# Performance work log

Measured on AMD Instinct MI355X. Metric: run time of the kernel, lower is better.

The kernel has to match this reference:

```python
import jax, jax.numpy as jnp
import numpy as np

TEMPERATURE = 1.0  # config['attention_temperature']


def setup_inputs() -> dict:
    key = jax.random.key(0)
    k1, k2, k3 = jax.random.split(key, 3)
    B, S, F, D = 4, 4096, 33, 64
    x = jax.random.normal(k1, (B, S, F), dtype=jnp.float32)
    Wq = jax.random.normal(k2, (F, D), dtype=jnp.float32) / np.sqrt(F)
    bq = jnp.zeros((D,), dtype=jnp.float32)
    Wk = jax.random.normal(k3, (F, D), dtype=jnp.float32) / np.sqrt(F)
    bk = jnp.zeros((D,), dtype=jnp.float32)
    return {"x": x, "Wq": Wq, "bq": bq, "Wk": Wk, "bk": bk}


def reference(x, Wq, bq, Wk, bk):
    # queries/keys: affine projections of the same input (MLP with one layer)
    q = x @ Wq + bq                              # [B, S, D]
    k = x @ Wk + bk                              # [B, S, D]
    qkt = jnp.einsum("bsd,btd->bst", q, k)       # [B, S, S]
    # non-standard normalization: divide each row by its max, scale by temperature
    row_max = jnp.max(qkt, axis=-1, keepdims=True)
    dist = jax.nn.softmax(TEMPERATURE * qkt / row_max, axis=-1)
    return dist
```

## Files before the change

kernel.cpp:

```cpp
#include <hip/hip_runtime.h>
#include <hip/hip_bf16.h>

typedef __bf16 bf16_t;
typedef __bf16 bf16x8 __attribute__((ext_vector_type(8)));
typedef float f32x4 __attribute__((ext_vector_type(4)));
typedef __fp16 f16x2 __attribute__((ext_vector_type(2)));

#define BATCH 4
#define SEQ 4096
#define FIN 33
#define DIM 64
#define LOG2E 1.4426950408889634f

__device__ __forceinline__ float dexp2(float x) { return __builtin_amdgcn_exp2f(x); }
__device__ __forceinline__ unsigned pk(float a, float b)
{ return __builtin_bit_cast(unsigned, __builtin_amdgcn_cvt_pkrtz(a, b)); }
__device__ __forceinline__ f16x2 uph(unsigned u)
{ return __builtin_bit_cast(f16x2, u); }
__device__ __forceinline__ float f16lo(unsigned u)
{ return (float)uph(u)[0]; }

__device__ __forceinline__ f32x4 mm2(bf16x8 a0, bf16x8 a1, bf16x8 b0, bf16x8 b1)
{
    f32x4 acc = {0.f, 0.f, 0.f, 0.f};
    acc = __builtin_amdgcn_mfma_f32_16x16x32_bf16(a0, b0, acc, 0, 0, 0);
    acc = __builtin_amdgcn_mfma_f32_16x16x32_bf16(a1, b1, acc, 0, 0, 0);
    return acc;
}

__global__ __launch_bounds__(256) void qk_proj_kernel(
    const float* __restrict__ x, const float* __restrict__ Wq,
    const float* __restrict__ bq, const float* __restrict__ Wk,
    const float* __restrict__ bk,
    bf16_t* __restrict__ qout, bf16_t* __restrict__ kout)
{
    __shared__ float sWq[FIN * DIM];
    __shared__ float sWk[FIN * DIM];
    __shared__ float sb[2 * DIM];
    const int t = threadIdx.x;
    for (int i = t; i < FIN * DIM; i += 256) { sWq[i] = Wq[i]; sWk[i] = Wk[i]; }
    if (t < DIM) { sb[t] = bq[t]; sb[DIM + t] = bk[t]; }
    __syncthreads();

    const int row = blockIdx.x * 4 + (t >> 6);
    const int d   = t & 63;
    const float* xr = x + (size_t)row * FIN;
    float qacc = sb[d], kacc = sb[DIM + d];
#pragma unroll
    for (int f = 0; f < FIN; ++f) {
        const float xv = xr[f];
        qacc += xv * sWq[f * DIM + d];
        kacc += xv * sWk[f * DIM + d];
    }
    qout[(size_t)row * DIM + d] = (bf16_t)qacc;
    kout[(size_t)row * DIM + d] = (bf16_t)kacc;
}

#define LDK(ct, h) (*reinterpret_cast<const bf16x8*>(kw + (size_t)(ct) * 16 * DIM + (h) * 32))

__global__ __launch_bounds__(256) void mz_kernel(
    const bf16_t* __restrict__ qg, const bf16_t* __restrict__ kg,
    float* __restrict__ cMg, float* __restrict__ invZg)
{
    const int wg   = blockIdx.x;
    const int b    = wg >> 7;
    const int t    = threadIdx.x;
    const int w    = t >> 6;
    const int l    = t & 63;
    const int lr   = l & 15;
    const int kg4  = l >> 4;
    const int col0 = w << 10;

    const bf16_t* kw = kg + ((size_t)b * SEQ + col0 + lr) * DIM + kg4 * 8;
    const bf16_t* qb = qg + (size_t)(wg * 32) * DIM;

    const bf16x8 qa0 = *reinterpret_cast<const bf16x8*>(qb + lr * DIM + kg4 * 8);
    const bf16x8 qa1 = *reinterpret_cast<const bf16x8*>(qb + lr * DIM + 32 + kg4 * 8);
    const bf16x8 qb0 = *reinterpret_cast<const bf16x8*>(qb + (16 + lr) * DIM + kg4 * 8);
    const bf16x8 qb1 = *reinterpret_cast<const bf16x8*>(qb + (16 + lr) * DIM + 32 + kg4 * 8);

    __shared__ float redM[4][32];
    __shared__ float redZ[4][32];

    float vA[4] = {-3.4e38f, -3.4e38f, -3.4e38f, -3.4e38f};
    float vB[4] = {-3.4e38f, -3.4e38f, -3.4e38f, -3.4e38f};
    {
        bf16x8 p0a = LDK(0, 0), p0b = LDK(0, 1);
        bf16x8 p1a = LDK(1, 0), p1b = LDK(1, 1);
#pragma unroll 4
        for (int ct = 0; ct < 64; ct += 2) {
            f32x4 aA = mm2(qa0, qa1, p0a, p0b);
            f32x4 aB = mm2(qb0, qb1, p0a, p0b);
            if (ct + 2 < 64) { p0a = LDK(ct + 2, 0); p0b = LDK(ct + 2, 1); }
#pragma unroll
            for (int j = 0; j < 4; ++j) { vA[j] = fmaxf(vA[j], aA[j]); vB[j] = fmaxf(vB[j], aB[j]); }
            f32x4 cA = mm2(qa0, qa1, p1a, p1b);
            f32x4 cB = mm2(qb0, qb1, p1a, p1b);
            if (ct + 3 < 64) { p1a = LDK(ct + 3, 0); p1b = LDK(ct + 3, 1); }
#pragma unroll
            for (int j = 0; j < 4; ++j) { vA[j] = fmaxf(vA[j], cA[j]); vB[j] = fmaxf(vB[j], cB[j]); }
        }
    }
#pragma unroll
    for (int m = 1; m < 16; m <<= 1) {
#pragma unroll
        for (int j = 0; j < 4; ++j) {
            vA[j] = fmaxf(vA[j], __shfl_xor(vA[j], m, 64));
            vB[j] = fmaxf(vB[j], __shfl_xor(vB[j], m, 64));
        }
    }
    if (lr == 0) {
#pragma unroll
        for (int j = 0; j < 4; ++j) {
            redM[w][kg4 * 4 + j]      = vA[j];
            redM[w][16 + kg4 * 4 + j] = vB[j];
        }
    }
    __syncthreads();
    float cMA[4], cMB[4];
#pragma unroll
    for (int j = 0; j < 4; ++j) {
        const int rA = kg4 * 4 + j, rB = 16 + kg4 * 4 + j;
        float mA = redM[0][rA], mB = redM[0][rB];
#pragma unroll
        for (int ww = 1; ww < 4; ++ww) { mA = fmaxf(mA, redM[ww][rA]); mB = fmaxf(mB, redM[ww][rB]); }
        cMA[j] = LOG2E / mA;
        cMB[j] = LOG2E / mB;
    }

    float zA[4] = {0.f, 0.f, 0.f, 0.f};
    float zB[4] = {0.f, 0.f, 0.f, 0.f};
    {
        bf16x8 p0a = LDK(0, 0), p0b = LDK(0, 1);
        bf16x8 p1a = LDK(1, 0), p1b = LDK(1, 1);
#pragma unroll 4
        for (int ct = 0; ct < 64; ct += 2) {
            f32x4 aA = mm2(qa0, qa1, p0a, p0b);
            f32x4 aB = mm2(qb0, qb1, p0a, p0b);
            if (ct + 2 < 64) { p0a = LDK(ct + 2, 0); p0b = LDK(ct + 2, 1); }
#pragma unroll
            for (int j = 0; j < 4; ++j) {
                zA[j] += dexp2(fmaf(aA[j], cMA[j], -LOG2E));
                zB[j] += dexp2(fmaf(aB[j], cMB[j], -LOG2E));
            }
            f32x4 cA = mm2(qa0, qa1, p1a, p1b);
            f32x4 cB = mm2(qb0, qb1, p1a, p1b);
            if (ct + 3 < 64) { p1a = LDK(ct + 3, 0); p1b = LDK(ct + 3, 1); }
#pragma unroll
            for (int j = 0; j < 4; ++j) {
                zA[j] += dexp2(fmaf(cA[j], cMA[j], -LOG2E));
                zB[j] += dexp2(fmaf(cB[j], cMB[j], -LOG2E));
            }
        }
    }
#pragma unroll
    for (int m = 1; m < 16; m <<= 1) {
#pragma unroll
        for (int j = 0; j < 4; ++j) {
            zA[j] += __shfl_xor(zA[j], m, 64);
            zB[j] += __shfl_xor(zB[j], m, 64);
        }
    }
    if (lr == 0) {
#pragma unroll
        for (int j = 0; j < 4; ++j) {
            redZ[w][kg4 * 4 + j]      = zA[j];
            redZ[w][16 + kg4 * 4 + j] = zB[j];
        }
    }
    __syncthreads();
    if (t < 32) {
        float mm = redM[0][t], zz = redZ[0][t];
#pragma unroll
        for (int ww = 1; ww < 4; ++ww) { mm = fmaxf(mm, redM[ww][t]); zz += redZ[ww][t]; }
        cMg[wg * 32 + t]   = LOG2E / mm;
        invZg[wg * 32 + t] = 1.0f / zz;
    }
}

__global__ __launch_bounds__(256) void p_kernel(
    const bf16_t* __restrict__ qg, const bf16_t* __restrict__ kg,
    const float* __restrict__ cMg, const float* __restrict__ invZg,
    float* __restrict__ out)
{
    const int w     = threadIdx.x >> 6;
    const int chunk = blockIdx.x * 4 + w;
    const int rb    = chunk >> 4;
    const int cc    = chunk & 15;
    const int b     = rb >> 8;
    const int l     = threadIdx.x & 63;
    const int lr    = l & 15;
    const int kg4   = l >> 4;
    const int col0  = cc << 8;
    const int sr    = l >> 3;

    __shared__ uint2 sS[4][4][256];
    uint2* const sp = &sS[w][kg4][lr];

    float cM[4];
#pragma unroll
    for (int j = 0; j < 4; ++j) cM[j] = cMg[rb * 16 + kg4 * 4 + j];
    const float iz0 = invZg[rb * 16 + sr];
    const float iz1 = invZg[rb * 16 + sr + 8];

    const bf16_t* qb = qg + (size_t)(rb * 16) * DIM;
    const bf16x8 a0 = *reinterpret_cast<const bf16x8*>(qb + lr * DIM + kg4 * 8);
    const bf16x8 a1 = *reinterpret_cast<const bf16x8*>(qb + lr * DIM + 32 + kg4 * 8);
    const bf16_t* kw = kg + ((size_t)b * SEQ + col0 + lr) * DIM + kg4 * 8;

    {
        bf16x8 p0a = LDK(0, 0), p0b = LDK(0, 1);
        bf16x8 p1a = LDK(1, 0), p1b = LDK(1, 1);
#pragma unroll
        for (int ct = 0; ct < 16; ct += 2) {
            f32x4 acc0 = mm2(a0, a1, p0a, p0b);
            if (ct + 2 < 16) { p0a = LDK(ct + 2, 0); p0b = LDK(ct + 2, 1); }
            {
                const float e0 = dexp2(fmaf(acc0[0], cM[0], -LOG2E));
                const float e1 = dexp2(fmaf(acc0[1], cM[1], -LOG2E));
                const float e2 = dexp2(fmaf(acc0[2], cM[2], -LOG2E));
                const float e3 = dexp2(fmaf(acc0[3], cM[3], -LOG2E));
                sp[ct * 16] = make_uint2(pk(e0, e1), pk(e2, e3));
            }
            f32x4 acc1 = mm2(a0, a1, p1a, p1b);
            if (ct + 3 < 16) { p1a = LDK(ct + 3, 0); p1b = LDK(ct + 3, 1); }
            {
                const float e0 = dexp2(fmaf(acc1[0], cM[0], -LOG2E));
                const float e1 = dexp2(fmaf(acc1[1], cM[1], -LOG2E));
                const float e2 = dexp2(fmaf(acc1[2], cM[2], -LOG2E));
                const float e3 = dexp2(fmaf(acc1[3], cM[3], -LOG2E));
                sp[(ct + 1) * 16] = make_uint2(pk(e0, e1), pk(e2, e3));
            }
        }
    }
    asm volatile("s_waitcnt lgkmcnt(0)" ::: "memory");

    {
        const int  cl  = (l & 7) * 4;
        const unsigned hsh = (unsigned)((sr & 1) * 16);
        const bool hiw = (sr & 2) != 0;
        const int  g0  = sr >> 2;
        float* ob0 = out + ((size_t)(rb * 16 + sr)) * SEQ + col0;
        float* ob1 = ob0 + (size_t)8 * SEQ;
#pragma unroll
        for (int it = 0; it < 8; ++it) {
            const int c = it * 32 + cl;
            const uint4 A0 = *reinterpret_cast<const uint4*>(&sS[w][g0][c]);
            const uint4 B0 = *reinterpret_cast<const uint4*>(&sS[w][g0][c + 2]);
            const uint4 A1 = *reinterpret_cast<const uint4*>(&sS[w][g0 + 2][c]);
            const uint4 B1 = *reinterpret_cast<const uint4*>(&sS[w][g0 + 2][c + 2]);
            f32x4 v0, v1;
            v0[0] = f16lo((hiw ? A0.y : A0.x) >> hsh);
            v0[1] = f16lo((hiw ? A0.w : A0.z) >> hsh);
            v0[2] = f16lo((hiw ? B0.y : B0.x) >> hsh);
            v0[3] = f16lo((hiw ? B0.w : B0.z) >> hsh);
            v1[0] = f16lo((hiw ? A1.y : A1.x) >> hsh);
            v1[1] = f16lo((hiw ? A1.w : A1.z) >> hsh);
            v1[2] = f16lo((hiw ? B1.y : B1.x) >> hsh);
            v1[3] = f16lo((hiw ? B1.w : B1.z) >> hsh);
            *reinterpret_cast<f32x4*>(ob0 + c) = v0 * iz0;
            *reinterpret_cast<f32x4*>(ob1 + c) = v1 * iz1;
        }
    }
}

extern "C" void kernel_launch(void* const* d_in, const int* in_sizes, int n_in,
                              void* d_out, int out_size, void* d_ws, size_t ws_size,
                              hipStream_t stream)
{
    const float* x  = (const float*)d_in[0];
    const float* Wq = (const float*)d_in[1];
    const float* bq = (const float*)d_in[2];
    const float* Wk = (const float*)d_in[3];
    const float* bk = (const float*)d_in[4];
    float* out = (float*)d_out;

    bf16_t* qws = (bf16_t*)d_ws;
    bf16_t* kws = qws + (size_t)BATCH * SEQ * DIM;
    float*  cMg = (float*)(kws + (size_t)BATCH * SEQ * DIM);
    float*  iZg = cMg + (size_t)BATCH * SEQ;

    qk_proj_kernel<<<(BATCH * SEQ) / 4, 256, 0, stream>>>(x, Wq, bq, Wk, bk, qws, kws);
    mz_kernel<<<BATCH * (SEQ / 32), 256, 0, stream>>>(qws, kws, cMg, iZg);
    p_kernel<<<BATCH * (SEQ / 16) * 16 / 4, 256, 0, stream>>>(qws, kws, cMg, iZg, out);
}
```

Before: 154.3 us.

## Halve rows per stats block, widen output blocks, and swizzle block order across XCDs

The max/sum kernel now handles 16 query rows per workgroup instead of 32, which doubles the grid and roughly halves per-block MFMA work. The output kernel uses 512-thread blocks that each cover half a row block (2048 columns across 8 waves). Its write-back now reads from shared memory across waves after a block barrier, so each wave writes two full contiguous rows. Both kernels remap blockIdx so consecutive blocks land on different XCDs while adjacent row blocks stay together for K reuse in L2. The trade-off is more K reloads in the stats pass and a full-block barrier in the output pass.

Result: slower. 208.4 us (+35.1%).

```diff
diff --git a/kernel.cpp b/kernel.cpp
--- a/kernel.cpp
+++ b/kernel.cpp
@@ -62,8 +62,8 @@
     const bf16_t* __restrict__ qg, const bf16_t* __restrict__ kg,
     float* __restrict__ cMg, float* __restrict__ invZg)
 {
-    const int wg   = blockIdx.x;
-    const int b    = wg >> 7;
+    const int wg   = ((blockIdx.x & 7) << 7) | (blockIdx.x >> 3);
+    const int b    = wg >> 8;
     const int t    = threadIdx.x;
     const int w    = t >> 6;
     const int l    = t & 63;
@@ -72,141 +72,110 @@
     const int col0 = w << 10;
 
     const bf16_t* kw = kg + ((size_t)b * SEQ + col0 + lr) * DIM + kg4 * 8;
-    const bf16_t* qb = qg + (size_t)(wg * 32) * DIM;
-
-    const bf16x8 qa0 = *reinterpret_cast<const bf16x8*>(qb + lr * DIM + kg4 * 8);
-    const bf16x8 qa1 = *reinterpret_cast<const bf16x8*>(qb + lr * DIM + 32 + kg4 * 8);
-    const bf16x8 qb0 = *reinterpret_cast<const bf16x8*>(qb + (16 + lr) * DIM + kg4 * 8);
-    const bf16x8 qb1 = *reinterpret_cast<const bf16x8*>(qb + (16 + lr) * DIM + 32 + kg4 * 8);
-
-    __shared__ float redM[4][32];
-    __shared__ float redZ[4][32];
-
-    float vA[4] = {-3.4e38f, -3.4e38f, -3.4e38f, -3.4e38f};
-    float vB[4] = {-3.4e38f, -3.4e38f, -3.4e38f, -3.4e38f};
+    const bf16_t* qb = qg + (size_t)(wg * 16) * DIM;
+
+    const bf16x8 a0 = *reinterpret_cast<const bf16x8*>(qb + lr * DIM + kg4 * 8);
+    const bf16x8 a1 = *reinterpret_cast<const bf16x8*>(qb + lr * DIM + 32 + kg4 * 8);
+
+    __shared__ float redM[4][16];
+    __shared__ float redZ[4][16];
+
+    float vmax[4] = {-3.4e38f, -3.4e38f, -3.4e38f, -3.4e38f};
     {
         bf16x8 p0a = LDK(0, 0), p0b = LDK(0, 1);
         bf16x8 p1a = LDK(1, 0), p1b = LDK(1, 1);
 #pragma unroll 4
         for (int ct = 0; ct < 64; ct += 2) {
-            f32x4 aA = mm2(qa0, qa1, p0a, p0b);
-            f32x4 aB = mm2(qb0, qb1, p0a, p0b);
+            f32x4 acc0 = mm2(a0, a1, p0a, p0b);
             if (ct + 2 < 64) { p0a = LDK(ct + 2, 0); p0b = LDK(ct + 2, 1); }
 #pragma unroll
-            for (int j = 0; j < 4; ++j) { vA[j] = fmaxf(vA[j], aA[j]); vB[j] = fmaxf(vB[j], aB[j]); }
-            f32x4 cA = mm2(qa0, qa1, p1a, p1b);
-            f32x4 cB = mm2(qb0, qb1, p1a, p1b);
+            for (int j = 0; j < 4; ++j) vmax[j] = fmaxf(vmax[j], acc0[j]);
+            f32x4 acc1 = mm2(a0, a1, p1a, p1b);
             if (ct + 3 < 64) { p1a = LDK(ct + 3, 0); p1b = LDK(ct + 3, 1); }
 #pragma unroll
-            for (int j = 0; j < 4; ++j) { vA[j] = fmaxf(vA[j], cA[j]); vB[j] = fmaxf(vB[j], cB[j]); }
+            for (int j = 0; j < 4; ++j) vmax[j] = fmaxf(vmax[j], acc1[j]);
         }
     }
 #pragma unroll
     for (int m = 1; m < 16; m <<= 1) {
 #pragma unroll
-        for (int j = 0; j < 4; ++j) {
-            vA[j] = fmaxf(vA[j], __shfl_xor(vA[j], m, 64));
-            vB[j] = fmaxf(vB[j], __shfl_xor(vB[j], m, 64));
-        }
+        for (int j = 0; j < 4; ++j) vmax[j] = fmaxf(vmax[j], __shfl_xor(vmax[j], m, 64));
     }
     if (lr == 0) {
 #pragma unroll
-        for (int j = 0; j < 4; ++j) {
-            redM[w][kg4 * 4 + j]      = vA[j];
-            redM[w][16 + kg4 * 4 + j] = vB[j];
-        }
-    }
-    __syncthreads();
-    float cMA[4], cMB[4];
+        for (int j = 0; j < 4; ++j) redM[w][kg4 * 4 + j] = vmax[j];
+    }
+    __syncthreads();
+    float cM[4];
 #pragma unroll
     for (int j = 0; j < 4; ++j) {
-        const int rA = kg4 * 4 + j, rB = 16 + kg4 * 4 + j;
-        float mA = redM[0][rA], mB = redM[0][rB];
-#pragma unroll
-        for (int ww = 1; ww < 4; ++ww) { mA = fmaxf(mA, redM[ww][rA]); mB = fmaxf(mB, redM[ww][rB]); }
-        cMA[j] = LOG2E / mA;
-        cMB[j] = LOG2E / mB;
-    }
-
-    float zA[4] = {0.f, 0.f, 0.f, 0.f};
-    float zB[4] = {0.f, 0.f, 0.f, 0.f};
+        const int r = kg4 * 4 + j;
+        const float mm = fmaxf(fmaxf(redM[0][r], redM[1][r]), fmaxf(redM[2][r], redM[3][r]));
+        cM[j] = LOG2E / mm;
+    }
+
+    float vsum[4] = {0.f, 0.f, 0.f, 0.f};
     {
         bf16x8 p0a = LDK(0, 0), p0b = LDK(0, 1);
         bf16x8 p1a = LDK(1, 0), p1b = LDK(1, 1);
 #pragma unroll 4
         for (int ct = 0; ct < 64; ct += 2) {
-            f32x4 aA = mm2(qa0, qa1, p0a, p0b);
-            f32x4 aB = mm2(qb0, qb1, p0a, p0b);
+            f32x4 acc0 = mm2(a0, a1, p0a, p0b);
             if (ct + 2 < 64) { p0a = LDK(ct + 2, 0); p0b = LDK(ct + 2, 1); }
 #pragma unroll
-            for (int j = 0; j < 4; ++j) {
-                zA[j] += dexp2(fmaf(aA[j], cMA[j], -LOG2E));
-                zB[j] += dexp2(fmaf(aB[j], cMB[j], -LOG2E));
-            }
-            f32x4 cA = mm2(qa0, qa1, p1a, p1b);
-            f32x4 cB = mm2(qb0, qb1, p1a, p1b);
+            for (int j = 0; j < 4; ++j) vsum[j] += dexp2(fmaf(acc0[j], cM[j], -LOG2E));
+            f32x4 acc1 = mm2(a0, a1, p1a, p1b);
             if (ct + 3 < 64) { p1a = LDK(ct + 3, 0); p1b = LDK(ct + 3, 1); }
 #pragma unroll
-            for (int j = 0; j < 4; ++j) {
-                zA[j] += dexp2(fmaf(cA[j], cMA[j], -LOG2E));
-                zB[j] += dexp2(fmaf(cB[j], cMB[j], -LOG2E));
-            }
+            for (int j = 0; j < 4; ++j) vsum[j] += dexp2(fmaf(acc1[j], cM[j], -LOG2E));
         }
     }
 #pragma unroll
     for (int m = 1; m < 16; m <<= 1) {
 #pragma unroll
-        for (int j = 0; j < 4; ++j) {
-            zA[j] += __shfl_xor(zA[j], m, 64);
-            zB[j] += __shfl_xor(zB[j], m, 64);
-        }
+        for (int j = 0; j < 4; ++j) vsum[j] += __shfl_xor(vsum[j], m, 64);
     }
     if (lr == 0) {
 #pragma unroll
-        for (int j = 0; j < 4; ++j) {
-            redZ[w][kg4 * 4 + j]      = zA[j];
-            redZ[w][16 + kg4 * 4 + j] = zB[j];
-        }
-    }
-    __syncthreads();
-    if (t < 32) {
-        float mm = redM[0][t], zz = redZ[0][t];
-#pragma unroll
-        for (int ww = 1; ww < 4; ++ww) { mm = fmaxf(mm, redM[ww][t]); zz += redZ[ww][t]; }
-        cMg[wg * 32 + t]   = LOG2E / mm;
-        invZg[wg * 32 + t] = 1.0f / zz;
-    }
-}
-
-__global__ __launch_bounds__(256) void p_kernel(
+        for (int j = 0; j < 4; ++j) redZ[w][kg4 * 4 + j] = vsum[j];
+    }
+    __syncthreads();
+    if (t < 16) {
+        const float mm = fmaxf(fmaxf(redM[0][t], redM[1][t]), fmaxf(redM[2][t], redM[3][t]));
+        const float zz = redZ[0][t] + redZ[1][t] + redZ[2][t] + redZ[3][t];
+        cMg[wg * 16 + t]   = LOG2E / mm;
+        invZg[wg * 16 + t] = 1.0f / zz;
+    }
+}
+
+__global__ __launch_bounds__(512) void p_kernel(
     const bf16_t* __restrict__ qg, const bf16_t* __restrict__ kg,
     const float* __restrict__ cMg, const float* __restrict__ invZg,
     float* __restrict__ out)
 {
-    const int w     = threadIdx.x >> 6;
-    const int chunk = blockIdx.x * 4 + w;
-    const int rb    = chunk >> 4;
-    const int cc    = chunk & 15;
-    const int b     = rb >> 8;
-    const int l     = threadIdx.x & 63;
-    const int lr    = l & 15;
-    const int kg4   = l >> 4;
-    const int col0  = cc << 8;
-    const int sr    = l >> 3;
-
-    __shared__ uint2 sS[4][4][256];
-    uint2* const sp = &sS[w][kg4][lr];
+    const int wgid = ((blockIdx.x & 7) << 8) | (blockIdx.x >> 3);
+    const int rb   = wgid >> 1;
+    const int half = wgid & 1;
+    const int b    = rb >> 8;
+    const int t    = threadIdx.x;
+    const int w    = t >> 6;
+    const int l    = t & 63;
+    const int lr   = l & 15;
+    const int kg4  = l >> 4;
+    const int col0 = half * 2048 + w * 256;
+
+    __shared__ uint2 sS[8][4][256];
 
     float cM[4];
 #pragma unroll
     for (int j = 0; j < 4; ++j) cM[j] = cMg[rb * 16 + kg4 * 4 + j];
-    const float iz0 = invZg[rb * 16 + sr];
-    const float iz1 = invZg[rb * 16 + sr + 8];
 
     const bf16_t* qb = qg + (size_t)(rb * 16) * DIM;
     const bf16x8 a0 = *reinterpret_cast<const bf16x8*>(qb + lr * DIM + kg4 * 8);
     const bf16x8 a1 = *reinterpret_cast<const bf16x8*>(qb + lr * DIM + 32 + kg4 * 8);
     const bf16_t* kw = kg + ((size_t)b * SEQ + col0 + lr) * DIM + kg4 * 8;
+
+    uint2* const sp = &sS[w][kg4][lr];
 
     {
         bf16x8 p0a = LDK(0, 0), p0b = LDK(0, 1);
@@ -233,33 +202,30 @@
             }
         }
     }
-    asm volatile("s_waitcnt lgkmcnt(0)" ::: "memory");
-
-    {
-        const int  cl  = (l & 7) * 4;
-        const unsigned hsh = (unsigned)((sr & 1) * 16);
-        const bool hiw = (sr & 2) != 0;
-        const int  g0  = sr >> 2;
-        float* ob0 = out + ((size_t)(rb * 16 + sr)) * SEQ + col0;
-        float* ob1 = ob0 + (size_t)8 * SEQ;
+    __syncthreads();
+
+    {
+        const int rA = 2 * w;
+        const int g  = w >> 1;
+        const bool useY = (w & 1);
+        const float izA = invZg[rb * 16 + rA];
+        const float izB = invZg[rb * 16 + rA + 1];
+        float* obA = out + ((size_t)(rb * 16 + rA)) * SEQ + half * 2048;
+        float* obB = obA + SEQ;
 #pragma unroll
         for (int it = 0; it < 8; ++it) {
-            const int c = it * 32 + cl;
-            const uint4 A0 = *reinterpret_cast<const uint4*>(&sS[w][g0][c]);
-            const uint4 B0 = *reinterpret_cast<const uint4*>(&sS[w][g0][c + 2]);
-            const uint4 A1 = *reinterpret_cast<const uint4*>(&sS[w][g0 + 2][c]);
-            const uint4 B1 = *reinterpret_cast<const uint4*>(&sS[w][g0 + 2][c + 2]);
-            f32x4 v0, v1;
-            v0[0] = f16lo((hiw ? A0.y : A0.x) >> hsh);
-            v0[1] = f16lo((hiw ? A0.w : A0.z) >> hsh);
-            v0[2] = f16lo((hiw ? B0.y : B0.x) >> hsh);
-            v0[3] = f16lo((hiw ? B0.w : B0.z) >> hsh);
-            v1[0] = f16lo((hiw ? A1.y : A1.x) >> hsh);
-            v1[1] = f16lo((hiw ? A1.w : A1.z) >> hsh);
-            v1[2] = f16lo((hiw ? B1.y : B1.x) >> hsh);
-            v1[3] = f16lo((hiw ? B1.w : B1.z) >> hsh);
-            *reinterpret_cast<f32x4*>(ob0 + c) = v0 * iz0;
-            *reinterpret_cast<f32x4*>(ob1 + c) = v1 * iz1;
+            const uint4 U0 = *reinterpret_cast<const uint4*>(&sS[it][g][4 * l]);
+            const uint4 U1 = *reinterpret_cast<const uint4*>(&sS[it][g][4 * l + 2]);
+            const unsigned w0 = useY ? U0.y : U0.x;
+            const unsigned w1 = useY ? U0.w : U0.z;
+            const unsigned w2 = useY ? U1.y : U1.x;
+            const unsigned w3 = useY ? U1.w : U1.z;
+            f32x4 vA, vB;
+            vA[0] = f16lo(w0); vA[1] = f16lo(w1); vA[2] = f16lo(w2); vA[3] = f16lo(w3);
+            vB[0] = f16lo(w0 >> 16); vB[1] = f16lo(w1 >> 16);
+            vB[2] = f16lo(w2 >> 16); vB[3] = f16lo(w3 >> 16);
+            *reinterpret_cast<f32x4*>(obA + it * 256 + 4 * l) = vA * izA;
+            *reinterpret_cast<f32x4*>(obB + it * 256 + 4 * l) = vB * izB;
         }
     }
 }
@@ -281,6 +247,6 @@
     float*  iZg = cMg + (size_t)BATCH * SEQ;
 
     qk_proj_kernel<<<(BATCH * SEQ) / 4, 256, 0, stream>>>(x, Wq, bq, Wk, bk, qws, kws);
-    mz_kernel<<<BATCH * (SEQ / 32), 256, 0, stream>>>(qws, kws, cMg, iZg);
-    p_kernel<<<BATCH * (SEQ / 16) * 16 / 4, 256, 0, stream>>>(qws, kws, cMg, iZg, out);
-}
+    mz_kernel<<<BATCH * (SEQ / 16), 256, 0, stream>>>(qws, kws, cMg, iZg);
+    p_kernel<<<BATCH * (SEQ / 16) * 2, 512, 0, stream>>>(qws, kws, cMg, iZg, out);
+}
```
